# Optimization experiments

Measured on AMD Instinct MI355X. Metric: run time of the kernel, lower is better.

Reference implementation:

```python
import jax, jax.numpy as jnp
import numpy as np

H = 256    # hidden_size
CVQ = 64   # vq_ph_channel
K = 128    # vq_ph_codebook_dim
NL = 5     # num_layers per ConvBlocks
NB = 2     # layers_in_block
KS = 3     # kernel_size


def _ln_c(x, g, b, eps=1e-5):
    # LayerNorm over channel dim of a [B, C, T] tensor
    m = jnp.mean(x, axis=1, keepdims=True)
    v = jnp.mean((x - m) ** 2, axis=1, keepdims=True)
    return (x - m) * jax.lax.rsqrt(v + eps) * g[None, :, None] + b[None, :, None]


def _causal_conv(x, w, b):
    # x [B,Cin,T], w [Cout,Cin,K]; left (causal) padding of K-1
    y = jax.lax.conv_general_dilated(x, w, (1,), [(w.shape[-1] - 1, 0)],
                                     dimension_numbers=('NCH', 'OIH', 'NCH'))
    return y + b[None, :, None]


def _pw(x, w, b):
    # pointwise (kernel-size-1) conv: w [Cout, Cin]
    return jnp.einsum('oi,bit->bot', w, x) + b[None, :, None]


def _conv_blocks(x, mask, ln_g, ln_b, w1, b1, w2, b2, last_g, last_b, post_w, post_b):
    # LeftPadConvBlocks: NL residual blocks x NB sub-blocks of
    # LN -> causal conv (C->2C, k=3) -> *k^-0.5 -> GELU -> 1x1 conv (2C->C), residual + mask
    scale = KS ** -0.5
    for i in range(NL):
        for j in range(NB):
            h = _ln_c(x, ln_g[i, j], ln_b[i, j])
            h = _causal_conv(h, w1[i, j], b1[i, j]) * scale
            h = jax.nn.gelu(h, approximate=False)
            h = _pw(h, w2[i, j], b2[i, j])
            x = (x + h) * mask
    x = _ln_c(x, last_g, last_b) * mask
    x = _causal_conv(x, post_w, post_b) * mask
    return x


def _group_by_segs(h_bct, mel2ph, L):
    # scatter-mean mel frames into phoneme segments; index 0 = padding (dropped)
    h = jnp.swapaxes(h_bct, 1, 2)  # [B, T, H]
    def one(hb, mb):
        s = jnp.zeros((L + 1, hb.shape[-1]), hb.dtype).at[mb].add(hb)
        c = jnp.zeros((L + 1,), hb.dtype).at[mb].add(1.0)
        return s[1:] / jnp.clip(c[1:], 1.0)[:, None]
    g = jax.vmap(one)(h, mel2ph)   # [B, L, H]
    return jnp.swapaxes(g, 1, 2)   # [B, H, L]


def _vq(z, codebook, beta=0.25):
    # EMA-VQ forward math: nearest-codebook lookup + straight-through + commitment loss
    x = jnp.swapaxes(z, 1, 2)                                # [B, T, C]
    d = (jnp.sum(x ** 2, -1, keepdims=True)
         - 2.0 * jnp.einsum('btc,kc->btk', x, codebook)
         + jnp.sum(codebook ** 2, -1))                       # [B, T, K]
    idx = jnp.argmin(d, axis=-1)                             # [B, T]
    q = codebook[idx]                                        # [B, T, C]
    loss = beta * jnp.mean((x - jax.lax.stop_gradient(q)) ** 2)
    q_st = x + jax.lax.stop_gradient(q - x)
    return jnp.swapaxes(q_st, 1, 2), loss, idx


def setup_inputs() -> dict:
    key = jax.random.key(0)
    ks = list(jax.random.split(key, 64))
    it = iter(ks)
    B, T, L = 16, 2048, 512
    f = lambda shape, s: jax.random.normal(next(it), shape, jnp.float32) * s
    inp = {}
    inp['x'] = jax.random.normal(next(it), (B, 80, T), jnp.float32)
    inp['in_nonpadding'] = jnp.ones((B, 1, T), jnp.float32)
    inp['in_mel2ph'] = jnp.sort(jax.random.randint(next(it), (B, T), 1, L + 1), axis=-1)
    inp['ph_nonpadding'] = jnp.ones((B, 1, L), jnp.float32)
    inp['conv_in_w'] = f((H, 80), 0.05)
    inp['conv_in_b'] = jnp.zeros((H,), jnp.float32)
    for p in ('enc', 'pn'):
        inp[p + '_ln_g'] = jnp.ones((NL, NB, H), jnp.float32)
        inp[p + '_ln_b'] = jnp.zeros((NL, NB, H), jnp.float32)
        inp[p + '_w1'] = f((NL, NB, 2 * H, H, KS), 0.03)
        inp[p + '_b1'] = jnp.zeros((NL, NB, 2 * H), jnp.float32)
        inp[p + '_w2'] = f((NL, NB, H, 2 * H), 0.03)
        inp[p + '_b2'] = jnp.zeros((NL, NB, H), jnp.float32)
        inp[p + '_last_g'] = jnp.ones((H,), jnp.float32)
        inp[p + '_last_b'] = jnp.zeros((H,), jnp.float32)
        inp[p + '_post_w'] = f((H, H, KS), 0.03)
        inp[p + '_post_b'] = jnp.zeros((H,), jnp.float32)
    inp['proj_in_w'] = f((CVQ, H), 0.05)
    inp['proj_in_b'] = jnp.zeros((CVQ,), jnp.float32)
    inp['proj_out_w'] = f((H, CVQ), 0.05)
    inp['proj_out_b'] = jnp.zeros((H,), jnp.float32)
    inp['codebook'] = f((K, CVQ), 0.1)
    return inp


def reference(x, in_nonpadding, in_mel2ph, ph_nonpadding,
              conv_in_w, conv_in_b,
              enc_ln_g, enc_ln_b, enc_w1, enc_b1, enc_w2, enc_b2,
              enc_last_g, enc_last_b, enc_post_w, enc_post_b,
              pn_ln_g, pn_ln_b, pn_w1, pn_b1, pn_w2, pn_b2,
              pn_last_g, pn_last_b, pn_post_w, pn_post_b,
              proj_in_w, proj_in_b, proj_out_w, proj_out_b, codebook):
    L = ph_nonpadding.shape[-1]
    h = _pw(x, conv_in_w, conv_in_b) * in_nonpadding                     # ph_conv_in
    h = _conv_blocks(h, in_nonpadding, enc_ln_g, enc_ln_b, enc_w1, enc_b1,
                     enc_w2, enc_b2, enc_last_g, enc_last_b,
                     enc_post_w, enc_post_b) * in_nonpadding             # ph_encoder
    h = _group_by_segs(h, in_mel2ph, L)                                  # [B, H, L]
    h = _conv_blocks(h, ph_nonpadding, pn_ln_g, pn_ln_b, pn_w1, pn_b1,
                     pn_w2, pn_b2, pn_last_g, pn_last_b,
                     pn_post_w, pn_post_b) * ph_nonpadding               # ph_postnet
    z = _pw(h, proj_in_w, proj_in_b)                                     # ph_latents_proj_in
    q, vq_loss, idx = _vq(z, codebook)                                   # VQ
    out = _pw(q, proj_out_w, proj_out_b)                                 # ph_latents_proj_out
    return out, vq_loss, idx
```

## Files before the change

kernel.cpp:

```cpp
#include <hip/hip_runtime.h>
#include <hip/hip_bf16.h>


typedef unsigned short u16;
typedef unsigned int u32;
typedef __attribute__((ext_vector_type(8))) _Float16 f16x8;
typedef __attribute__((ext_vector_type(16))) float f32x16;

#define OUT_LOSS_OFF 2097152
#define OUT_IDX_OFF  2097153

__device__ __forceinline__ void split_f16(float x, u16& h, u16& l) {
    union { _Float16 f; u16 u; } a, b;
    a.f = (_Float16)x;
    float hf = (float)a.f;
    b.f = (_Float16)(x - hf);
    h = a.u; l = b.u;
}

__global__ __launch_bounds__(256) void k_t_mat(const float* __restrict__ w,
                                               float* __restrict__ wt,
                                               int G, int O, int I) {
    size_t n = (size_t)G * O * I;
    for (size_t i = (size_t)blockIdx.x * 256 + threadIdx.x; i < n;
         i += (size_t)gridDim.x * 256) {
        int ci = (int)(i % I);
        int o  = (int)((i / I) % O);
        int g  = (int)(i / ((size_t)I * O));
        wt[((size_t)g * I + ci) * O + o] = w[i];
    }
}

__global__ __launch_bounds__(256) void k_t_w1mf(const float* __restrict__ w,
                                                u16* __restrict__ BH,
                                                u16* __restrict__ BL, int S) {
    size_t N = (size_t)S * 3 * 16 * 16 * 64 * 8;
    for (size_t i = (size_t)blockIdx.x * 256 + threadIdx.x; i < N;
         i += (size_t)gridDim.x * 256) {
        int j = (int)(i & 7); size_t r = i >> 3;
        int L = (int)(r & 63); r >>= 6;
        int nt = (int)(r & 15); r >>= 4;
        int kb = (int)(r & 15); r >>= 4;
        int k3 = (int)(r % 3); int s = (int)(r / 3);
        int oc = nt * 32 + (L & 31);
        int c = kb * 16 + ((L >> 5) << 3) + j;
        float v = w[(((size_t)s * 512 + oc) * 256 + c) * 3 + k3];
        u16 h, l; split_f16(v, h, l);
        BH[i] = h; BL[i] = l;
    }
}

__global__ __launch_bounds__(256) void k_t_w2mf(const float* __restrict__ w,
                                                u16* __restrict__ BH,
                                                u16* __restrict__ BL, int S) {
    size_t N = (size_t)S * 32 * 8 * 64 * 8;
    for (size_t i = (size_t)blockIdx.x * 256 + threadIdx.x; i < N;
         i += (size_t)gridDim.x * 256) {
        int j = (int)(i & 7);
        int L = (int)((i >> 3) & 63);
        int nt = (int)((i >> 9) & 7);
        int kb = (int)((i >> 12) & 31);
        int s = (int)(i >> 17);
        int oc = nt * 32 + (L & 31);
        int ic = kb * 16 + ((L >> 5) << 3) + j;
        float v = w[((size_t)s * 256 + oc) * 512 + ic];
        u16 h, l; split_f16(v, h, l);
        BH[i] = h; BL[i] = l;
    }
}

__global__ __launch_bounds__(256) void k_t_wpmf(const float* __restrict__ w,
                                                u16* __restrict__ BH,
                                                u16* __restrict__ BL) {
    int i = blockIdx.x * 256 + threadIdx.x;
    int j = i & 7;
    int L = (i >> 3) & 63;
    int nt = (i >> 9) & 7;
    int kb = (i >> 12) & 15;
    int k3 = i >> 16;
    int oc = nt * 32 + (L & 31);
    int c = kb * 16 + ((L >> 5) << 3) + j;
    float v = w[((size_t)oc * 256 + c) * 3 + k3];
    u16 h, l; split_f16(v, h, l);
    BH[i] = h; BL[i] = l;
}

template <int CIN, int COUT, int CHUNK, bool STATS>
__global__ __launch_bounds__(256) void k_pw(const float* __restrict__ x,
                                            const float* __restrict__ wt,
                                            const float* __restrict__ bias,
                                            const float* __restrict__ mask,
                                            float* __restrict__ y,
                                            float* __restrict__ MM,
                                            float* __restrict__ IV, int T) {
    extern __shared__ float X[];
    constexpr int NG = COUT / CHUNK;
    __shared__ float rs[64 * NG], rs2[64 * NG];
    const int b = blockIdx.y, t0 = blockIdx.x * 64;
    for (int i = threadIdx.x; i < CIN * 64; i += 256) {
        int ci = i >> 6, j = i & 63;
        X[i] = x[((size_t)b * CIN + ci) * T + t0 + j];
    }
    __syncthreads();
    const int tl = threadIdx.x & 63;
    const int g = __builtin_amdgcn_readfirstlane((int)(threadIdx.x >> 6));
    float acc[CHUNK];
#pragma unroll
    for (int o = 0; o < CHUNK; o++) acc[o] = 0.f;
    for (int i = 0; i < CIN; i++) {
        float xv = X[i * 64 + tl];
        const float* wr = wt + (size_t)i * COUT + g * CHUNK;
#pragma unroll
        for (int o = 0; o < CHUNK; o++) acc[o] = fmaf(wr[o], xv, acc[o]);
    }
    float mk = mask ? mask[(size_t)b * T + t0 + tl] : 1.0f;
    float s = 0.f, s2 = 0.f;
#pragma unroll
    for (int o = 0; o < CHUNK; o++) {
        int oc = g * CHUNK + o;
        float val = (acc[o] + bias[oc]) * mk;
        y[((size_t)b * COUT + oc) * T + t0 + tl] = val;
        s += val; s2 += val * val;
    }
    if constexpr (STATS) {
        rs[g * 64 + tl] = s; rs2[g * 64 + tl] = s2;
        __syncthreads();
        if (threadIdx.x < 64) {
            float ss = 0.f, ss2 = 0.f;
#pragma unroll
            for (int gg = 0; gg < NG; gg++) {
                ss += rs[gg * 64 + threadIdx.x];
                ss2 += rs2[gg * 64 + threadIdx.x];
            }
            float m = ss * (1.0f / COUT);
            float var = ss2 * (1.0f / COUT) - m * m;
            MM[(size_t)b * T + t0 + threadIdx.x] = m;
            IV[(size_t)b * T + t0 + threadIdx.x] = 1.0f / sqrtf(var + 1e-5f);
        }
    }
}

__global__ __launch_bounds__(512, 4) void k_sub(
    const float* __restrict__ xin, float* __restrict__ xout,
    const float* __restrict__ MMi, const float* __restrict__ IVi,
    const float* __restrict__ lng, const float* __restrict__ lnb,
    const u16* __restrict__ B1H, const u16* __restrict__ B1L,
    const float* __restrict__ b1,
    const u16* __restrict__ B2H, const u16* __restrict__ B2L,
    const float* __restrict__ b2, const float* __restrict__ mask,
    float* __restrict__ MMo, float* __restrict__ IVo, int T) {
    __shared__ __align__(16) char smem[73280];
    u16* LH = (u16*)smem;
    u16* LL = (u16*)(smem + 17952);
    u32* G  = (u32*)(smem + 35904);
    float* SOUT = (float*)smem;
    float* rs  = (float*)(smem + 69184);
    float* rs2 = (float*)(smem + 71232);

    const int tid = threadIdx.x;
    const int b = blockIdx.y, t0 = blockIdx.x * 32;
    const size_t xoff = (size_t)b * 256 * T;
    const size_t bT = (size_t)b * T;

    {
        int jj = tid & 31;
        int cg = tid >> 5;
        int t = t0 - 2 + jj;
        bool ok = (t >= 0);
        float m = ok ? MMi[bT + t] : 0.f;
        float v = ok ? IVi[bT + t] : 0.f;
#pragma unroll
        for (int i = 0; i < 16; i++) {
            int c = cg + i * 16;
            float xv = ok ? xin[xoff + (size_t)c * T + t] : 0.f;
            float ln = ok ? ((xv - m) * v * lng[c] + lnb[c]) : 0.f;
            u16 h, l; split_f16(ln, h, l);
            LH[jj * 264 + c] = h; LL[jj * 264 + c] = l;
        }
        int j2 = 32 + (tid >> 8);
        int c2 = tid & 255;
        int t2 = t0 + 30 + (tid >> 8);
        float m2 = MMi[bT + t2], v2 = IVi[bT + t2];
        float x2 = xin[xoff + (size_t)c2 * T + t2];
        float ln2 = (x2 - m2) * v2 * lng[c2] + lnb[c2];
        u16 h2, l2; split_f16(ln2, h2, l2);
        LH[j2 * 264 + c2] = h2; LL[j2 * 264 + c2] = l2;
    }
    __syncthreads();

    const int lane = tid & 63;
    const int w = tid >> 6;
    const int arow = lane & 31;
    const int acol = (lane >> 5) << 3;
    const int thalf = (lane >> 5) << 2;
    const float ks = 0.5773502691896258f;
    const int oc_l = w * 32 + (lane & 31);
    const u16* b1h0 = B1H + (size_t)w * 512 + (size_t)lane * 8;
    const u16* b1l0 = B1L + (size_t)w * 512 + (size_t)lane * 8;
    const u16* b1h1 = B1H + (size_t)(8 + w) * 512 + (size_t)lane * 8;
    const u16* b1l1 = B1L + (size_t)(8 + w) * 512 + (size_t)lane * 8;
    const u16* b2h = B2H + (size_t)w * 512 + (size_t)lane * 8;
    const u16* b2l = B2L + (size_t)w * 512 + (size_t)lane * 8;
    const int grow = (lane & 31) * 260;

    f32x16 c2H, c2M;
#pragma unroll
    for (int r = 0; r < 16; r++) { c2H[r] = 0.f; c2M[r] = 0.f; }

    f32x16 aH, aM;
#pragma unroll
    for (int r = 0; r < 16; r++) { aH[r] = 0.f; aM[r] = 0.f; }
#pragma unroll
    for (int kk = 0; kk < 48; kk++) {
        int k3 = kk >> 4, kb = kk & 15;
        int ao = (arow + k3) * 264 + kb * 16 + acol;
        f16x8 ah = *(const f16x8*)&LH[ao];
        f16x8 al = *(const f16x8*)&LL[ao];
        f16x8 bh = *(const f16x8*)(b1h0 + (size_t)kk * 8192);
        f16x8 bl = *(const f16x8*)(b1l0 + (size_t)kk * 8192);
        aH = __builtin_amdgcn_mfma_f32_32x32x16_f16(ah, bh, aH, 0, 0, 0);
        aM = __builtin_amdgcn_mfma_f32_32x32x16_f16(ah, bl, aM, 0, 0, 0);
        aM = __builtin_amdgcn_mfma_f32_32x32x16_f16(al, bh, aM, 0, 0, 0);
    }
    {
        float bb = b1[oc_l];
#pragma unroll
        for (int r = 0; r < 16; r++) {
            int trow = thalf + ((r >> 2) << 3) + (r & 3);
            float y = (aH[r] + aM[r] + bb) * ks;
            float ge = 0.5f * y * (1.0f + erff(y * 0.7071067811865476f));
            u16 h, l; split_f16(ge, h, l);
            G[trow * 260 + oc_l] = ((u32)h << 16) | (u32)l;
        }
    }
    __syncthreads();

#pragma unroll
    for (int r = 0; r < 16; r++) { aH[r] = 0.f; aM[r] = 0.f; }
    for (int i = 0; i < 16; i++) {
#pragma unroll
        for (int t3 = 0; t3 < 3; t3++) {
            int kk = i * 3 + t3;
            int k3 = kk >> 4, kb = kk & 15;
            int ao = (arow + k3) * 264 + kb * 16 + acol;
            f16x8 ah = *(const f16x8*)&LH[ao];
            f16x8 al = *(const f16x8*)&LL[ao];
            f16x8 bh = *(const f16x8*)(b1h1 + (size_t)kk * 8192);
            f16x8 bl = *(const f16x8*)(b1l1 + (size_t)kk * 8192);
            aH = __builtin_amdgcn_mfma_f32_32x32x16_f16(ah, bh, aH, 0, 0, 0);
            aM = __builtin_amdgcn_mfma_f32_32x32x16_f16(ah, bl, aM, 0, 0, 0);
            aM = __builtin_amdgcn_mfma_f32_32x32x16_f16(al, bh, aM, 0, 0, 0);
        }
        {
            const u32* gp = &G[grow + i * 16 + acol];
            uint4 p0 = *(const uint4*)gp;
            uint4 p1 = *(const uint4*)(gp + 4);
            union { f16x8 v; u32 u[4]; } gh, gl;
            gh.u[0] = __builtin_amdgcn_perm(p0.y, p0.x, 0x07060302u);
            gl.u[0] = __builtin_amdgcn_perm(p0.y, p0.x, 0x05040100u);
            gh.u[1] = __builtin_amdgcn_perm(p0.w, p0.z, 0x07060302u);
            gl.u[1] = __builtin_amdgcn_perm(p0.w, p0.z, 0x05040100u);
            gh.u[2] = __builtin_amdgcn_perm(p1.y, p1.x, 0x07060302u);
            gl.u[2] = __builtin_amdgcn_perm(p1.y, p1.x, 0x05040100u);
            gh.u[3] = __builtin_amdgcn_perm(p1.w, p1.z, 0x07060302u);
            gl.u[3] = __builtin_amdgcn_perm(p1.w, p1.z, 0x05040100u);
            f16x8 bh = *(const f16x8*)(b2h + (size_t)i * 4096);
            f16x8 bl = *(const f16x8*)(b2l + (size_t)i * 4096);
            c2H = __builtin_amdgcn_mfma_f32_32x32x16_f16(gh.v, bh, c2H, 0, 0, 0);
            c2M = __builtin_amdgcn_mfma_f32_32x32x16_f16(gh.v, bl, c2M, 0, 0, 0);
            c2M = __builtin_amdgcn_mfma_f32_32x32x16_f16(gl.v, bh, c2M, 0, 0, 0);
        }
    }
    __syncthreads();
    {
        float bb = b1[256 + oc_l];
#pragma unroll
        for (int r = 0; r < 16; r++) {
            int trow = thalf + ((r >> 2) << 3) + (r & 3);
            float y = (aH[r] + aM[r] + bb) * ks;
            float ge = 0.5f * y * (1.0f + erff(y * 0.7071067811865476f));
            u16 h, l; split_f16(ge, h, l);
            G[trow * 260 + oc_l] = ((u32)h << 16) | (u32)l;
        }
    }
    __syncthreads();

    for (int i = 0; i < 16; i++) {
        const u32* gp = &G[grow + i * 16 + acol];
        uint4 p0 = *(const uint4*)gp;
        uint4 p1 = *(const uint4*)(gp + 4);
        union { f16x8 v; u32 u[4]; } gh, gl;
        gh.u[0] = __builtin_amdgcn_perm(p0.y, p0.x, 0x07060302u);
        gl.u[0] = __builtin_amdgcn_perm(p0.y, p0.x, 0x05040100u);
        gh.u[1] = __builtin_amdgcn_perm(p0.w, p0.z, 0x07060302u);
        gl.u[1] = __builtin_amdgcn_perm(p0.w, p0.z, 0x05040100u);
        gh.u[2] = __builtin_amdgcn_perm(p1.y, p1.x, 0x07060302u);
        gl.u[2] = __builtin_amdgcn_perm(p1.y, p1.x, 0x05040100u);
        gh.u[3] = __builtin_amdgcn_perm(p1.w, p1.z, 0x07060302u);
        gl.u[3] = __builtin_amdgcn_perm(p1.w, p1.z, 0x05040100u);
        f16x8 bh = *(const f16x8*)(b2h + (size_t)(16 + i) * 4096);
        f16x8 bl = *(const f16x8*)(b2l + (size_t)(16 + i) * 4096);
        c2H = __builtin_amdgcn_mfma_f32_32x32x16_f16(gh.v, bh, c2H, 0, 0, 0);
        c2M = __builtin_amdgcn_mfma_f32_32x32x16_f16(gh.v, bl, c2M, 0, 0, 0);
        c2M = __builtin_amdgcn_mfma_f32_32x32x16_f16(gl.v, bh, c2M, 0, 0, 0);
    }
#pragma unroll
    for (int r = 0; r < 16; r++) {
        int trow = thalf + ((r >> 2) << 3) + (r & 3);
        SOUT[trow * 260 + oc_l] = c2H[r] + c2M[r];
    }
    __syncthreads();
    {
        int t = tid & 31, cg = tid >> 5;
        float mk = mask[bT + t0 + t];
        float s = 0.f, s2 = 0.f;
#pragma unroll
        for (int i = 0; i < 16; i++) {
            int c = cg * 16 + i;
            size_t adr = xoff + (size_t)c * T + t0 + t;
            float val = (xin[adr] + SOUT[t * 260 + c] + b2[c]) * mk;
            xout[adr] = val;
            s += val; s2 += val * val;
        }
        rs[tid] = s; rs2[tid] = s2;
    }
    __syncthreads();
    if (tid < 32) {
        float ss = 0.f, ss2 = 0.f;
#pragma unroll
        for (int k = 0; k < 16; k++) {
            ss += rs[k * 32 + tid]; ss2 += rs2[k * 32 + tid];
        }
        float m = ss * (1.0f / 256.0f);
        float var = ss2 * (1.0f / 256.0f) - m * m;
        MMo[bT + t0 + tid] = m;
        IVo[bT + t0 + tid] = 1.0f / sqrtf(var + 1e-5f);
    }
}

__global__ __launch_bounds__(512, 8) void k_lnc(
    const float* __restrict__ xin, float* __restrict__ xout,
    const float* __restrict__ MM, const float* __restrict__ IV,
    const float* __restrict__ lg, const float* __restrict__ lb,
    const u16* __restrict__ BH, const u16* __restrict__ BL,
    const float* __restrict__ bias, const float* __restrict__ mask, int T) {
    __shared__ __align__(16) char smem[35904];
    u16* LH = (u16*)smem;
    u16* LL = (u16*)(smem + 17952);
    float* SOUT = (float*)smem;

    const int tid = threadIdx.x;
    const int b = blockIdx.y, t0 = blockIdx.x * 32;
    const size_t xoff = (size_t)b * 256 * T;
    const size_t bT = (size_t)b * T;

    {
        int jj = tid & 31;
        int cg = tid >> 5;
        int t = t0 - 2 + jj;
        bool ok = (t >= 0);
        float m = ok ? MM[bT + t] : 0.f;
        float v = ok ? IV[bT + t] : 0.f;
        float mk = ok ? mask[bT + t] : 0.f;
#pragma unroll
        for (int i = 0; i < 16; i++) {
            int c = cg + i * 16;
            float xv = ok ? xin[xoff + (size_t)c * T + t] : 0.f;
            float ln = ok ? ((xv - m) * v * lg[c] + lb[c]) * mk : 0.f;
            u16 h, l; split_f16(ln, h, l);
            LH[jj * 264 + c] = h; LL[jj * 264 + c] = l;
        }
        int j2 = 32 + (tid >> 8);
        int c2 = tid & 255;
        int t2 = t0 + 30 + (tid >> 8);
        float ln2 = ((xin[xoff + (size_t)c2 * T + t2] - MM[bT + t2]) *
                     IV[bT + t2] * lg[c2] + lb[c2]) * mask[bT + t2];
        u16 h2, l2; split_f16(ln2, h2, l2);
        LH[j2 * 264 + c2] = h2; LL[j2 * 264 + c2] = l2;
    }
    __syncthreads();

    const int lane = tid & 63;
    const int w = tid >> 6;
    const int arow = lane & 31;
    const int acol = (lane >> 5) << 3;
    const int thalf = (lane >> 5) << 2;
    const u16* bph = BH + (size_t)w * 512 + (size_t)lane * 8;
    const u16* bpl = BL + (size_t)w * 512 + (size_t)lane * 8;

    f32x16 aH, aM;
#pragma unroll
    for (int r = 0; r < 16; r++) { aH[r] = 0.f; aM[r] = 0.f; }
    for (int kk = 0; kk < 48; kk++) {
        int k3 = kk >> 4, kb = kk & 15;
        int ao = (arow + k3) * 264 + kb * 16 + acol;
        f16x8 ah = *(const f16x8*)&LH[ao];
        f16x8 al = *(const f16x8*)&LL[ao];
        f16x8 bh = *(const f16x8*)(bph + (size_t)kk * 4096);
        f16x8 bl = *(const f16x8*)(bpl + (size_t)kk * 4096);
        aH = __builtin_amdgcn_mfma_f32_32x32x16_f16(ah, bh, aH, 0, 0, 0);
        aM = __builtin_amdgcn_mfma_f32_32x32x16_f16(ah, bl, aM, 0, 0, 0);
        aM = __builtin_amdgcn_mfma_f32_32x32x16_f16(al, bh, aM, 0, 0, 0);
    }
    __syncthreads();
    {
        int oc = w * 32 + (lane & 31);
#pragma unroll
        for (int r = 0; r < 16; r++) {
            int trow = thalf + ((r >> 2) << 3) + (r & 3);
            SOUT[trow * 260 + oc] = aH[r] + aM[r];
        }
    }
    __syncthreads();
    {
        int t = tid & 31, cg = tid >> 5;
        float mk = mask[bT + t0 + t];
#pragma unroll
        for (int i = 0; i < 16; i++) {
            int c = cg * 16 + i;
            xout[xoff + (size_t)c * T + t0 + t] =
                (SOUT[t * 260 + c] + bias[c]) * mk;
        }
    }
}

__global__ __launch_bounds__(256) void k_counts(const int* __restrict__ m2p,
                                                int* __restrict__ cnt) {
    __shared__ int c[512];
    int b = blockIdx.x;
    for (int i = threadIdx.x; i < 512; i += 256) c[i] = 0;
    __syncthreads();
    for (int t = threadIdx.x; t < 2048; t += 256) {
        int p = m2p[b * 2048 + t];
        if (p >= 1 && p <= 512) atomicAdd(&c[p - 1], 1);
    }
    __syncthreads();
    for (int i = threadIdx.x; i < 512; i += 256) cnt[b * 512 + i] = c[i];
}

__global__ __launch_bounds__(256) void k_scatter(const float* __restrict__ h,
                                                 const int* __restrict__ m2p,
                                                 float* __restrict__ g) {
    extern __shared__ float sm[];
    float* HT = sm;
    int* ph = (int*)(sm + 256 * 65);
    int b = blockIdx.y, t0 = blockIdx.x * 64;
    if (threadIdx.x < 64) ph[threadIdx.x] = m2p[b * 2048 + t0 + threadIdx.x];
    for (int i = threadIdx.x; i < 256 * 64; i += 256) {
        int c = i >> 6, j = i & 63;
        HT[c * 65 + j] = h[((size_t)b * 256 + c) * 2048 + t0 + j];
    }
    __syncthreads();
    int c = threadIdx.x;
    float run = 0.f;
    int cur = ph[0];
    for (int j = 0; j < 64; j++) {
        int p = ph[j];
        if (p != cur) {
            if (cur >= 1 && cur <= 512)
                atomicAdd(&g[((size_t)b * 256 + c) * 512 + cur - 1], run);
            run = 0.f;
            cur = p;
        }
        run += HT[c * 65 + j];
    }
    if (cur >= 1 && cur <= 512)
        atomicAdd(&g[((size_t)b * 256 + c) * 512 + cur - 1], run);
}

__global__ __launch_bounds__(512) void k_postprep(float* __restrict__ g,
                                                  const int* __restrict__ cnt,
                                                  float* __restrict__ MM,
                                                  float* __restrict__ IV) {
    int b = blockIdx.x, l = threadIdx.x;
    int c1 = cnt[b * 512 + l];
    if (c1 < 1) c1 = 1;
    float rc = 1.0f / (float)c1;
    float s = 0.f, s2 = 0.f;
    for (int c = 0; c < 256; c++) {
        size_t idx = ((size_t)b * 256 + c) * 512 + l;
        float v = g[idx] * rc;
        g[idx] = v;
        s += v; s2 += v * v;
    }
    float m = s * (1.0f / 256.0f);
    float var = s2 * (1.0f / 256.0f) - m * m;
    MM[(size_t)b * 512 + l] = m;
    IV[(size_t)b * 512 + l] = 1.0f / sqrtf(var + 1e-5f);
}

__global__ __launch_bounds__(256) void k_vq(const float* __restrict__ z,
                                            const float* __restrict__ cb,
                                            int* __restrict__ idxout,
                                            float* __restrict__ out,
                                            float* __restrict__ lossacc) {
    int n = blockIdx.x * 256 + threadIdx.x;
    int b = n >> 9, l = n & 511;
    float zr[64];
#pragma unroll
    for (int c = 0; c < 64; c++) zr[c] = z[((size_t)b * 64 + c) * 512 + l];
    float best = 3.4e38f;
    int bi = 0;
    for (int k = 0; k < 128; k++) {
        const float* cr = cb + k * 64;
        float d = 0.f;
#pragma unroll
        for (int c = 0; c < 64; c++) {
            float t = zr[c] - cr[c];
            d = fmaf(t, t, d);
        }
        if (d < best) { best = d; bi = k; }
    }
    idxout[n] = bi;
    out[OUT_IDX_OFF + n] = (float)bi;
    atomicAdd(lossacc, best);
}

__global__ void k_loss(const float* __restrict__ acc, float* __restrict__ out) {
    if (threadIdx.x == 0 && blockIdx.x == 0)
        out[OUT_LOSS_OFF] = 0.25f * acc[0] * (1.0f / 524288.0f);
}

__global__ __launch_bounds__(256) void k_projout(const float* __restrict__ cb,
                                                 const int* __restrict__ idx,
                                                 const float* __restrict__ wt,
                                                 const float* __restrict__ bias,
                                                 float* __restrict__ out) {
    __shared__ float Q[64 * 64];
    __shared__ int ids[64];
    int b = blockIdx.y, l0 = blockIdx.x * 64;
    if (threadIdx.x < 64) ids[threadIdx.x] = idx[b * 512 + l0 + threadIdx.x];
    __syncthreads();
    for (int i = threadIdx.x; i < 4096; i += 256) {
        int c = i >> 6, l = i & 63;
        Q[c * 64 + l] = cb[ids[l] * 64 + c];
    }
    __syncthreads();
    int tl = threadIdx.x & 63;
    int g = __builtin_amdgcn_readfirstlane((int)(threadIdx.x >> 6));
    float acc[64];
#pragma unroll
    for (int o = 0; o < 64; o++) acc[o] = 0.f;
    for (int i = 0; i < 64; i++) {
        float xv = Q[i * 64 + tl];
        const float* wr = wt + i * 256 + g * 64;
#pragma unroll
        for (int o = 0; o < 64; o++) acc[o] = fmaf(wr[o], xv, acc[o]);
    }
#pragma unroll
    for (int o = 0; o < 64; o++) {
        int oc = g * 64 + o;
        out[(size_t)b * 131072 + (size_t)oc * 512 + l0 + tl] = acc[o] + bias[oc];
    }
}

extern "C" void kernel_launch(void* const* d_in, const int* in_sizes, int n_in,
                              void* d_out, int out_size, void* d_ws, size_t ws_size,
                              hipStream_t stream) {
    (void)in_sizes; (void)n_in; (void)out_size; (void)ws_size;
    const float* x          = (const float*)d_in[0];
    const float* in_np      = (const float*)d_in[1];
    const int*   mel2ph     = (const int*)d_in[2];
    const float* ph_np      = (const float*)d_in[3];
    const float* conv_in_w  = (const float*)d_in[4];
    const float* conv_in_b  = (const float*)d_in[5];
    const float* e_ln_g = (const float*)d_in[6];
    const float* e_ln_b = (const float*)d_in[7];
    const float* e_w1   = (const float*)d_in[8];
    const float* e_b1   = (const float*)d_in[9];
    const float* e_w2   = (const float*)d_in[10];
    const float* e_b2   = (const float*)d_in[11];
    const float* e_lg   = (const float*)d_in[12];
    const float* e_lb   = (const float*)d_in[13];
    const float* e_pw   = (const float*)d_in[14];
    const float* e_pb   = (const float*)d_in[15];
    const float* p_ln_g = (const float*)d_in[16];
    const float* p_ln_b = (const float*)d_in[17];
    const float* p_w1   = (const float*)d_in[18];
    const float* p_b1   = (const float*)d_in[19];
    const float* p_w2   = (const float*)d_in[20];
    const float* p_b2   = (const float*)d_in[21];
    const float* p_lg   = (const float*)d_in[22];
    const float* p_lb   = (const float*)d_in[23];
    const float* p_pw   = (const float*)d_in[24];
    const float* p_pb   = (const float*)d_in[25];
    const float* proj_in_w  = (const float*)d_in[26];
    const float* proj_in_b  = (const float*)d_in[27];
    const float* proj_out_w = (const float*)d_in[28];
    const float* proj_out_b = (const float*)d_in[29];
    const float* codebook   = (const float*)d_in[30];
    float* out = (float*)d_out;

    float* ws = (float*)d_ws;
    float* A      = ws;
    float* Bb     = A + 8388608;
    float* CINT   = Bb + 8388608;
    float* PINT   = CINT + 20480;
    float* POUTT  = PINT + 16384;
    float* Z      = POUTT + 16384;
    float* MM0    = Z + 524288;
    float* IV0    = MM0 + 32768;
    float* MM1    = IV0 + 32768;
    float* IV1    = MM1 + 32768;
    int*   CNT    = (int*)(IV1 + 32768);
    int*   IDX    = CNT + 8192;
    float* LOSS   = (float*)(IDX + 8192);
    u16*   BH1E   = (u16*)(LOSS + 64);
    u16*   BL1E   = BH1E + 3932160;
    u16*   BH1P   = BL1E + 3932160;
    u16*   BL1P   = BH1P + 3932160;
    u16*   BH2E   = BL1P + 3932160;
    u16*   BL2E   = BH2E + 1310720;
    u16*   BH2P   = BL2E + 1310720;
    u16*   BL2P   = BH2P + 1310720;
    u16*   PH_E   = BL2P + 1310720;
    u16*   PL_E   = PH_E + 196608;
    u16*   PH_P   = PL_E + 196608;
    u16*   PL_P   = PH_P + 196608;

    k_t_w1mf<<<dim3(4096), dim3(256), 0, stream>>>(e_w1, BH1E, BL1E, 10);
    k_t_w1mf<<<dim3(4096), dim3(256), 0, stream>>>(p_w1, BH1P, BL1P, 10);
    k_t_w2mf<<<dim3(2048), dim3(256), 0, stream>>>(e_w2, BH2E, BL2E, 10);
    k_t_w2mf<<<dim3(2048), dim3(256), 0, stream>>>(p_w2, BH2P, BL2P, 10);
    k_t_wpmf<<<dim3(768),  dim3(256), 0, stream>>>(e_pw, PH_E, PL_E);
    k_t_wpmf<<<dim3(768),  dim3(256), 0, stream>>>(p_pw, PH_P, PL_P);
    k_t_mat  <<<dim3(80),  dim3(256), 0, stream>>>(conv_in_w, CINT, 1, 256, 80);
    k_t_mat  <<<dim3(64),  dim3(256), 0, stream>>>(proj_in_w, PINT, 1, 64, 256);
    k_t_mat  <<<dim3(64),  dim3(256), 0, stream>>>(proj_out_w, POUTT, 1, 256, 64);

    const size_t sm_scat = 256 * 65 * sizeof(float) + 64 * sizeof(int);

    k_pw<80, 256, 64, true><<<dim3(32, 16), dim3(256), 80 * 64 * 4, stream>>>(
        x, CINT, conv_in_b, in_np, A, MM0, IV0, 2048);

    float* cur = A;
    float* nxt = Bb;
    for (int s = 0; s < 10; s++) {
        float* mi = (s & 1) ? MM1 : MM0;
        float* vi = (s & 1) ? IV1 : IV0;
        float* mo = (s & 1) ? MM0 : MM1;
        float* vo = (s & 1) ? IV0 : IV1;
        k_sub<<<dim3(64, 16), dim3(512), 0, stream>>>(
            cur, nxt, mi, vi, e_ln_g + s * 256, e_ln_b + s * 256,
            BH1E + (size_t)s * 393216, BL1E + (size_t)s * 393216, e_b1 + s * 512,
            BH2E + (size_t)s * 131072, BL2E + (size_t)s * 131072, e_b2 + s * 256,
            in_np, mo, vo, 2048);
        float* t = cur; cur = nxt; nxt = t;
    }
    k_lnc<<<dim3(64, 16), dim3(512), 0, stream>>>(
        cur, nxt, MM0, IV0, e_lg, e_lb, PH_E, PL_E, e_pb, in_np, 2048);

    hipMemsetAsync(A, 0, (size_t)2097152 * 4, stream);
    hipMemsetAsync(LOSS, 0, 4, stream);
    k_counts<<<dim3(16), dim3(256), 0, stream>>>(mel2ph, CNT);
    k_scatter<<<dim3(32, 16), dim3(256), sm_scat, stream>>>(Bb, mel2ph, A);
    k_postprep<<<dim3(16), dim3(512), 0, stream>>>(A, CNT, MM0, IV0);

    cur = A; nxt = Bb;
    for (int s = 0; s < 10; s++) {
        float* mi = (s & 1) ? MM1 : MM0;
        float* vi = (s & 1) ? IV1 : IV0;
        float* mo = (s & 1) ? MM0 : MM1;
        float* vo = (s & 1) ? IV0 : IV1;
        k_sub<<<dim3(16, 16), dim3(512), 0, stream>>>(
            cur, nxt, mi, vi, p_ln_g + s * 256, p_ln_b + s * 256,
            BH1P + (size_t)s * 393216, BL1P + (size_t)s * 393216, p_b1 + s * 512,
            BH2P + (size_t)s * 131072, BL2P + (size_t)s * 131072, p_b2 + s * 256,
            ph_np, mo, vo, 512);
        float* t = cur; cur = nxt; nxt = t;
    }
    k_lnc<<<dim3(16, 16), dim3(512), 0, stream>>>(
        cur, nxt, MM0, IV0, p_lg, p_lb, PH_P, PL_P, p_pb, ph_np, 512);

    k_pw<256, 64, 16, false><<<dim3(8, 16), dim3(256), 256 * 64 * 4, stream>>>(
        Bb, PINT, proj_in_b, nullptr, Z, nullptr, nullptr, 512);

    k_vq<<<dim3(32), dim3(256), 0, stream>>>(Z, codebook, IDX, out, LOSS);
    k_loss<<<dim3(1), dim3(64), 0, stream>>>(LOSS, out);
    k_projout<<<dim3(8, 16), dim3(256), 0, stream>>>(codebook, IDX, POUTT,
                                                     proj_out_b, out);
}
```

Baseline: 2.334 ms.

## Restructure sub-block conv so both halves share A loads and reuse LDS

Computes both output halves of the causal conv in one loop, so each LDS A fragment is loaded once for two MFMA chains. This frees the separate G buffer: GELU output is stored as split f16 hi/lo planes over the LN region, which removes the perm unpacking and cuts shared memory roughly in half, and launch bounds rise to 6 blocks per CU. It also merges the hi/mid accumulators into one chain, adds s_setprio around MFMA loops and partially unrolls them. The cost is more live accumulators per wave, serial dependence on a single accumulator, and an extra barrier, so register pressure under the higher occupancy target could cause spills.

```diff
diff --git a/kernel.cpp b/kernel.cpp
--- a/kernel.cpp
+++ b/kernel.cpp
@@ -140,7 +140,7 @@
     }
 }
 
-__global__ __launch_bounds__(512, 4) void k_sub(
+__global__ __launch_bounds__(512, 6) void k_sub(
     const float* __restrict__ xin, float* __restrict__ xout,
     const float* __restrict__ MMi, const float* __restrict__ IVi,
     const float* __restrict__ lng, const float* __restrict__ lnb,
@@ -149,13 +149,14 @@
     const u16* __restrict__ B2H, const u16* __restrict__ B2L,
     const float* __restrict__ b2, const float* __restrict__ mask,
     float* __restrict__ MMo, float* __restrict__ IVo, int T) {
-    __shared__ __align__(16) char smem[73280];
+    __shared__ __align__(16) char smem[40128];
     u16* LH = (u16*)smem;
     u16* LL = (u16*)(smem + 17952);
-    u32* G  = (u32*)(smem + 35904);
+    u16* GH = (u16*)smem;
+    u16* GL = (u16*)(smem + 17952);
     float* SOUT = (float*)smem;
-    float* rs  = (float*)(smem + 69184);
-    float* rs2 = (float*)(smem + 71232);
+    float* rs  = (float*)(smem + 36032);
+    float* rs2 = (float*)(smem + 38080);
 
     const int tid = threadIdx.x;
     const int b = blockIdx.y, t0 = blockIdx.x * 32;
@@ -201,113 +202,93 @@
     const u16* b1l1 = B1L + (size_t)(8 + w) * 512 + (size_t)lane * 8;
     const u16* b2h = B2H + (size_t)w * 512 + (size_t)lane * 8;
     const u16* b2l = B2L + (size_t)w * 512 + (size_t)lane * 8;
-    const int grow = (lane & 31) * 260;
-
-    f32x16 c2H, c2M;
-#pragma unroll
-    for (int r = 0; r < 16; r++) { c2H[r] = 0.f; c2M[r] = 0.f; }
-
-    f32x16 aH, aM;
-#pragma unroll
-    for (int r = 0; r < 16; r++) { aH[r] = 0.f; aM[r] = 0.f; }
-#pragma unroll
+    const int grow = (lane & 31) * 264;
+
+    f32x16 c0, c1;
+#pragma unroll
+    for (int r = 0; r < 16; r++) { c0[r] = 0.f; c1[r] = 0.f; }
+    __builtin_amdgcn_s_setprio(1);
+#pragma unroll 4
     for (int kk = 0; kk < 48; kk++) {
         int k3 = kk >> 4, kb = kk & 15;
         int ao = (arow + k3) * 264 + kb * 16 + acol;
         f16x8 ah = *(const f16x8*)&LH[ao];
         f16x8 al = *(const f16x8*)&LL[ao];
-        f16x8 bh = *(const f16x8*)(b1h0 + (size_t)kk * 8192);
-        f16x8 bl = *(const f16x8*)(b1l0 + (size_t)kk * 8192);
-        aH = __builtin_amdgcn_mfma_f32_32x32x16_f16(ah, bh, aH, 0, 0, 0);
-        aM = __builtin_amdgcn_mfma_f32_32x32x16_f16(ah, bl, aM, 0, 0, 0);
-        aM = __builtin_amdgcn_mfma_f32_32x32x16_f16(al, bh, aM, 0, 0, 0);
-    }
+        f16x8 bh0 = *(const f16x8*)(b1h0 + (size_t)kk * 8192);
+        f16x8 bl0 = *(const f16x8*)(b1l0 + (size_t)kk * 8192);
+        f16x8 bh1 = *(const f16x8*)(b1h1 + (size_t)kk * 8192);
+        f16x8 bl1 = *(const f16x8*)(b1l1 + (size_t)kk * 8192);
+        c0 = __builtin_amdgcn_mfma_f32_32x32x16_f16(ah, bh0, c0, 0, 0, 0);
+        c1 = __builtin_amdgcn_mfma_f32_32x32x16_f16(ah, bh1, c1, 0, 0, 0);
+        c0 = __builtin_amdgcn_mfma_f32_32x32x16_f16(ah, bl0, c0, 0, 0, 0);
+        c1 = __builtin_amdgcn_mfma_f32_32x32x16_f16(ah, bl1, c1, 0, 0, 0);
+        c0 = __builtin_amdgcn_mfma_f32_32x32x16_f16(al, bh0, c0, 0, 0, 0);
+        c1 = __builtin_amdgcn_mfma_f32_32x32x16_f16(al, bh1, c1, 0, 0, 0);
+    }
+    __builtin_amdgcn_s_setprio(0);
+    __syncthreads();
+
     {
         float bb = b1[oc_l];
 #pragma unroll
         for (int r = 0; r < 16; r++) {
             int trow = thalf + ((r >> 2) << 3) + (r & 3);
-            float y = (aH[r] + aM[r] + bb) * ks;
+            float y = (c0[r] + bb) * ks;
             float ge = 0.5f * y * (1.0f + erff(y * 0.7071067811865476f));
             u16 h, l; split_f16(ge, h, l);
-            G[trow * 260 + oc_l] = ((u32)h << 16) | (u32)l;
-        }
-    }
-    __syncthreads();
-
-#pragma unroll
-    for (int r = 0; r < 16; r++) { aH[r] = 0.f; aM[r] = 0.f; }
+            GH[trow * 264 + oc_l] = h; GL[trow * 264 + oc_l] = l;
+        }
+    }
+    __syncthreads();
+
+    f32x16 c2acc;
+#pragma unroll
+    for (int r = 0; r < 16; r++) c2acc[r] = 0.f;
+    __builtin_amdgcn_s_setprio(1);
+#pragma unroll 4
     for (int i = 0; i < 16; i++) {
-#pragma unroll
-        for (int t3 = 0; t3 < 3; t3++) {
-            int kk = i * 3 + t3;
-            int k3 = kk >> 4, kb = kk & 15;
-            int ao = (arow + k3) * 264 + kb * 16 + acol;
-            f16x8 ah = *(const f16x8*)&LH[ao];
-            f16x8 al = *(const f16x8*)&LL[ao];
-            f16x8 bh = *(const f16x8*)(b1h1 + (size_t)kk * 8192);
-            f16x8 bl = *(const f16x8*)(b1l1 + (size_t)kk * 8192);
-            aH = __builtin_amdgcn_mfma_f32_32x32x16_f16(ah, bh, aH, 0, 0, 0);
-            aM = __builtin_amdgcn_mfma_f32_32x32x16_f16(ah, bl, aM, 0, 0, 0);
-            aM = __builtin_amdgcn_mfma_f32_32x32x16_f16(al, bh, aM, 0, 0, 0);
-        }
-        {
-            const u32* gp = &G[grow + i * 16 + acol];
-            uint4 p0 = *(const uint4*)gp;
-            uint4 p1 = *(const uint4*)(gp + 4);
-            union { f16x8 v; u32 u[4]; } gh, gl;
-            gh.u[0] = __builtin_amdgcn_perm(p0.y, p0.x, 0x07060302u);
-            gl.u[0] = __builtin_amdgcn_perm(p0.y, p0.x, 0x05040100u);
-            gh.u[1] = __builtin_amdgcn_perm(p0.w, p0.z, 0x07060302u);
-            gl.u[1] = __builtin_amdgcn_perm(p0.w, p0.z, 0x05040100u);
-            gh.u[2] = __builtin_amdgcn_perm(p1.y, p1.x, 0x07060302u);
-            gl.u[2] = __builtin_amdgcn_perm(p1.y, p1.x, 0x05040100u);
-            gh.u[3] = __builtin_amdgcn_perm(p1.w, p1.z, 0x07060302u);
-            gl.u[3] = __builtin_amdgcn_perm(p1.w, p1.z, 0x05040100u);
-            f16x8 bh = *(const f16x8*)(b2h + (size_t)i * 4096);
-            f16x8 bl = *(const f16x8*)(b2l + (size_t)i * 4096);
-            c2H = __builtin_amdgcn_mfma_f32_32x32x16_f16(gh.v, bh, c2H, 0, 0, 0);
-            c2M = __builtin_amdgcn_mfma_f32_32x32x16_f16(gh.v, bl, c2M, 0, 0, 0);
-            c2M = __builtin_amdgcn_mfma_f32_32x32x16_f16(gl.v, bh, c2M, 0, 0, 0);
-        }
-    }
-    __syncthreads();
+        f16x8 gh = *(const f16x8*)&GH[grow + i * 16 + acol];
+        f16x8 gl = *(const f16x8*)&GL[grow + i * 16 + acol];
+        f16x8 bh2 = *(const f16x8*)(b2h + (size_t)i * 4096);
+        f16x8 bl2 = *(const f16x8*)(b2l + (size_t)i * 4096);
+        c2acc = __builtin_amdgcn_mfma_f32_32x32x16_f16(gh, bh2, c2acc, 0, 0, 0);
+        c2acc = __builtin_amdgcn_mfma_f32_32x32x16_f16(gh, bl2, c2acc, 0, 0, 0);
+        c2acc = __builtin_amdgcn_mfma_f32_32x32x16_f16(gl, bh2, c2acc, 0, 0, 0);
+    }
+    __builtin_amdgcn_s_setprio(0);
+    __syncthreads();
+
     {
         float bb = b1[256 + oc_l];
 #pragma unroll
         for (int r = 0; r < 16; r++) {
             int trow = thalf + ((r >> 2) << 3) + (r & 3);
-            float y = (aH[r] + aM[r] + bb) * ks;
+            float y = (c1[r] + bb) * ks;
             float ge = 0.5f * y * (1.0f + erff(y * 0.7071067811865476f));
             u16 h, l; split_f16(ge, h, l);
-            G[trow * 260 + oc_l] = ((u32)h << 16) | (u32)l;
-        }
-    }
-    __syncthreads();
-
+            GH[trow * 264 + oc_l] = h; GL[trow * 264 + oc_l] = l;
+        }
+    }
+    __syncthreads();
+
+    __builtin_amdgcn_s_setprio(1);
+#pragma unroll 4
     for (int i = 0; i < 16; i++) {
-        const u32* gp = &G[grow + i * 16 + acol];
-        uint4 p0 = *(const uint4*)gp;
-        uint4 p1 = *(const uint4*)(gp + 4);
-        union { f16x8 v; u32 u[4]; } gh, gl;
-        gh.u[0] = __builtin_amdgcn_perm(p0.y, p0.x, 0x07060302u);
-        gl.u[0] = __builtin_amdgcn_perm(p0.y, p0.x, 0x05040100u);
-        gh.u[1] = __builtin_amdgcn_perm(p0.w, p0.z, 0x07060302u);
-        gl.u[1] = __builtin_amdgcn_perm(p0.w, p0.z, 0x05040100u);
-        gh.u[2] = __builtin_amdgcn_perm(p1.y, p1.x, 0x07060302u);
-        gl.u[2] = __builtin_amdgcn_perm(p1.y, p1.x, 0x05040100u);
-        gh.u[3] = __builtin_amdgcn_perm(p1.w, p1.z, 0x07060302u);
-        gl.u[3] = __builtin_amdgcn_perm(p1.w, p1.z, 0x05040100u);
-        f16x8 bh = *(const f16x8*)(b2h + (size_t)(16 + i) * 4096);
-        f16x8 bl = *(const f16x8*)(b2l + (size_t)(16 + i) * 4096);
-        c2H = __builtin_amdgcn_mfma_f32_32x32x16_f16(gh.v, bh, c2H, 0, 0, 0);
-        c2M = __builtin_amdgcn_mfma_f32_32x32x16_f16(gh.v, bl, c2M, 0, 0, 0);
-        c2M = __builtin_amdgcn_mfma_f32_32x32x16_f16(gl.v, bh, c2M, 0, 0, 0);
-    }
+        f16x8 gh = *(const f16x8*)&GH[grow + i * 16 + acol];
+        f16x8 gl = *(const f16x8*)&GL[grow + i * 16 + acol];
+        f16x8 bh2 = *(const f16x8*)(b2h + (size_t)(16 + i) * 4096);
+        f16x8 bl2 = *(const f16x8*)(b2l + (size_t)(16 + i) * 4096);
+        c2acc = __builtin_amdgcn_mfma_f32_32x32x16_f16(gh, bh2, c2acc, 0, 0, 0);
+        c2acc = __builtin_amdgcn_mfma_f32_32x32x16_f16(gh, bl2, c2acc, 0, 0, 0);
+        c2acc = __builtin_amdgcn_mfma_f32_32x32x16_f16(gl, bh2, c2acc, 0, 0, 0);
+    }
+    __builtin_amdgcn_s_setprio(0);
+    __syncthreads();
+
 #pragma unroll
     for (int r = 0; r < 16; r++) {
         int trow = thalf + ((r >> 2) << 3) + (r & 3);
-        SOUT[trow * 260 + oc_l] = c2H[r] + c2M[r];
+        SOUT[trow * 260 + oc_l] = c2acc[r];
     }
     __syncthreads();
     {
@@ -391,6 +372,8 @@
     f32x16 aH, aM;
 #pragma unroll
     for (int r = 0; r < 16; r++) { aH[r] = 0.f; aM[r] = 0.f; }
+    __builtin_amdgcn_s_setprio(1);
+#pragma unroll 4
     for (int kk = 0; kk < 48; kk++) {
         int k3 = kk >> 4, kb = kk & 15;
         int ao = (arow + k3) * 264 + kb * 16 + acol;
@@ -402,6 +385,7 @@
         aM = __builtin_amdgcn_mfma_f32_32x32x16_f16(ah, bl, aM, 0, 0, 0);
         aM = __builtin_amdgcn_mfma_f32_32x32x16_f16(al, bh, aM, 0, 0, 0);
     }
+    __builtin_amdgcn_s_setprio(0);
     __syncthreads();
     {
         int oc = w * 32 + (lane & 31);
```

Result: slower. 2.416 ms (+3.5%).
